# Performance work log

Hardware: AMD Instinct MI355X
Metric: run time of the kernel (lower is better)

Reference implementation:

```python
import jax, jax.numpy as jnp
import numpy as np

D_MODEL = 1024
N_HEADS = 16
HEAD_DIM = D_MODEL // N_HEADS  # 64
BATCH = 2
SEQ = 2048
THETA = 10000.0


def _rope_tables(theta, d_k, max_seq_len):
    # matches RoPE.__init__: d = theta**(2*arange(d_k//2)/d_k); t = s / d
    inv = theta ** (2.0 * jnp.arange(0, d_k // 2, dtype=jnp.float32) / d_k)  # [d_k//2]
    s = jnp.arange(max_seq_len, dtype=jnp.float32)[:, None]  # [S,1]
    t = s / inv[None, :]  # [S, d_k//2]
    return jnp.sin(t), jnp.cos(t)


def setup_inputs() -> dict:
    key = jax.random.key(0)
    ks = jax.random.split(key, 5)
    std = np.sqrt(2.0 / (D_MODEL + D_MODEL))
    x = jax.random.normal(ks[0], (BATCH, SEQ, D_MODEL), dtype=jnp.float32)
    Wq = jax.random.normal(ks[1], (D_MODEL, D_MODEL), dtype=jnp.float32) * std
    Wk = jax.random.normal(ks[2], (D_MODEL, D_MODEL), dtype=jnp.float32) * std
    Wv = jax.random.normal(ks[3], (D_MODEL, D_MODEL), dtype=jnp.float32) * std
    Wo = jax.random.normal(ks[4], (D_MODEL, D_MODEL), dtype=jnp.float32) * std
    token_positions = jnp.arange(SEQ, dtype=jnp.int64)
    rope_sin, rope_cos = _rope_tables(THETA, HEAD_DIM, SEQ)
    return {"x": x, "token_positions": token_positions, "Wq": Wq, "Wk": Wk,
            "Wv": Wv, "Wo": Wo, "rope_sin": rope_sin, "rope_cos": rope_cos}


def _apply_rope(x, sin, cos):
    # x: [B, H, S, d_k]; sin/cos: [S, d_k//2] (gathered by token_positions)
    x1 = x[..., ::2]
    x2 = x[..., 1::2]
    x_even = x1 * cos - x2 * sin
    x_odd = x1 * sin + x2 * cos
    # interleave back: stack on last dim then flatten
    return jnp.stack([x_even, x_odd], axis=-1).reshape(x.shape)


def reference(x, token_positions, Wq, Wk, Wv, Wo, rope_sin, rope_cos):
    b, s, _ = x.shape
    h, d = N_HEADS, HEAD_DIM

    def proj(W):
        y = jnp.einsum('oi,bsi->bso', W, x)
        return y.reshape(b, s, h, d).transpose(0, 2, 1, 3)  # [b, h, s, d]

    q = proj(Wq)
    k = proj(Wk)
    v = proj(Wv)

    sin = rope_sin[token_positions]  # [s, d//2]
    cos = rope_cos[token_positions]
    q = _apply_rope(q, sin, cos)
    k = _apply_rope(k, sin, cos)

    # causal scaled-dot-product attention (FlashAttention.apply(..., True))
    scale = 1.0 / jnp.sqrt(jnp.asarray(d, dtype=x.dtype))
    scores = jnp.einsum('bhqd,bhkd->bhqk', q, k) * scale
    causal = jnp.tril(jnp.ones((s, s), dtype=bool))
    scores = jnp.where(causal, scores, jnp.finfo(x.dtype).min)
    attn = jax.nn.softmax(scores, axis=-1)
    out = jnp.einsum('bhqk,bhkd->bhqd', attn, v)  # [b, h, s, d]
    out = out.transpose(0, 2, 1, 3).reshape(b, s, h * d)
    return jnp.einsum('oi,bsi->bso', Wo, out)
```

## Files before the change

kernel.cpp:

```cpp
#include <hip/hip_runtime.h>
#include <hip/hip_bf16.h>
#include <math.h>

#define BATCH   2
#define S_LEN   2048
#define DM      1024
#define NH      16
#define HD      64
#define MROWS   4096

typedef __hip_bfloat16 bf16;
typedef __attribute__((ext_vector_type(8))) short short8;
typedef __attribute__((ext_vector_type(4))) float float4v;

#define QSCALE 0.18033688011112043f

#define WC_VM0   0x0F70
#define WC_VM3   0x0F73
#define WC_VM4   0x0F74
#define WC_VM6   0x0F76
#define WC_VM8   0x0F78
#define WC_LGKM0 0xC07F

__device__ __forceinline__ short f2s(float x) {
    union { bf16 h; short s; } u; u.h = __float2bfloat16(x); return u.s;
}
__device__ __forceinline__ short8 load8(const void* p) {
    return *reinterpret_cast<const short8*>(p);
}
__device__ __forceinline__ void cvt8(const float* g, bf16* d) {
    float4v a = *reinterpret_cast<const float4v*>(g);
    float4v b = *reinterpret_cast<const float4v*>(g + 4);
    short8 r;
    r[0] = f2s(a[0]); r[1] = f2s(a[1]); r[2] = f2s(a[2]); r[3] = f2s(a[3]);
    r[4] = f2s(b[0]); r[5] = f2s(b[1]); r[6] = f2s(b[2]); r[7] = f2s(b[3]);
    *reinterpret_cast<short8*>(d) = r;
}
__device__ __forceinline__ void gll16(const void* g, void* l) {
    __builtin_amdgcn_global_load_lds(
        (const __attribute__((address_space(1))) unsigned int*)g,
        (__attribute__((address_space(3))) unsigned int*)l,
        16, 0, 0);
}
__device__ __forceinline__ unsigned pack2(float a, float b) {
    union { float f; unsigned u; } ua, ub;
    ua.f = a; ub.f = b;
    return ((ua.u + 0x8000u) >> 16) | ((ub.u + 0x8000u) & 0xFFFF0000u);
}

__global__ __launch_bounds__(256) void cvt_kernel(const float* __restrict__ x,
                                                  const float* __restrict__ wq,
                                                  const float* __restrict__ wk,
                                                  const float* __restrict__ wv,
                                                  const float* __restrict__ wo,
                                                  bf16* __restrict__ xb,
                                                  bf16* __restrict__ wqb,
                                                  bf16* __restrict__ wkb,
                                                  bf16* __restrict__ wvb,
                                                  bf16* __restrict__ wob) {
    const size_t i = ((size_t)blockIdx.x * 256 + threadIdx.x) * 8;
    const size_t NX = (size_t)MROWS * DM;
    const size_t NW = (size_t)DM * DM;
    if (i < NX)                { cvt8(x  + i,               xb  + i); }
    else if (i < NX + NW)      { cvt8(wq + (i - NX),        wqb + (i - NX)); }
    else if (i < NX + 2 * NW)  { cvt8(wk + (i - NX - NW),   wkb + (i - NX - NW)); }
    else if (i < NX + 3 * NW)  { cvt8(wv + (i - NX - 2*NW), wvb + (i - NX - 2*NW)); }
    else                       { cvt8(wo + (i - NX - 3*NW), wob + (i - NX - 3*NW)); }
}

__global__ __launch_bounds__(256) void qkv_gemm(const bf16* __restrict__ A,
                                                const bf16* __restrict__ Wqb,
                                                const bf16* __restrict__ Wkb,
                                                const bf16* __restrict__ Wvb,
                                                bf16* __restrict__ Qb, bf16* __restrict__ Kb,
                                                bf16* __restrict__ Vtb,
                                                const float* __restrict__ rsin,
                                                const float* __restrict__ rcos) {
    __shared__ short As[3][128 * 32];
    __shared__ short Bs[3][128 * 32];

    const int j    = threadIdx.x;
    const int w    = j >> 6;
    const int lane = j & 63;
    const int quad = lane >> 4;
    const int lid  = lane & 15;
    const int wm   = w & 1, wn = w >> 1;

    const int mb  = blockIdx.x * 128;
    const int sel = blockIdx.y >> 3;
    const int nb  = (blockIdx.y & 7) * 128;
    const bf16* W = (sel == 0) ? Wqb : (sel == 1) ? Wkb : Wvb;

    int sOff[2];
#pragma unroll
    for (int i = 0; i < 2; ++i) {
        const int idx = (i * 4 + w) * 64 + lane;
        const int r = idx >> 2;
        const int c = (idx & 3) ^ (r & 3) ^ ((r >> 2) & 3);
        sOff[i] = r * DM + c * 8;
    }
    const bf16* baseA = A + (size_t)mb * DM;
    const bf16* baseB = W + (size_t)nb * DM;

#pragma unroll
    for (int t = 0; t < 2; ++t) {
#pragma unroll
        for (int i = 0; i < 2; ++i) gll16(baseA + t * 32 + sOff[i], &As[t][(i * 4 + w) * 512]);
#pragma unroll
        for (int i = 0; i < 2; ++i) gll16(baseB + t * 32 + sOff[i], &Bs[t][(i * 4 + w) * 512]);
    }

    int aRd[4], bRd[4];
#pragma unroll
    for (int t = 0; t < 4; ++t) {
        const int ra = wm * 64 + t * 16 + lid;
        aRd[t] = ra * 32 + ((quad ^ (ra & 3) ^ ((ra >> 2) & 3)) * 8);
        const int rb = wn * 64 + t * 16 + lid;
        bRd[t] = rb * 32 + ((quad ^ (rb & 3) ^ ((rb >> 2) & 3)) * 8);
    }

    float4v acc[4][4] = {};
    int buf = 0;
    for (int it = 0; it < 32; ++it) {
        __builtin_amdgcn_s_barrier();
        if (it < 30) {
            const int k0 = (it + 2) * 32;
            const int b = (buf + 2 >= 3) ? buf - 1 : buf + 2;
#pragma unroll
            for (int i = 0; i < 2; ++i) gll16(baseA + k0 + sOff[i], &As[b][(i * 4 + w) * 512]);
#pragma unroll
            for (int i = 0; i < 2; ++i) gll16(baseB + k0 + sOff[i], &Bs[b][(i * 4 + w) * 512]);
            __builtin_amdgcn_s_waitcnt(WC_VM8);
        } else if (it == 30) {
            __builtin_amdgcn_s_waitcnt(WC_VM4);
        } else {
            __builtin_amdgcn_s_waitcnt(WC_VM0);
        }
        __builtin_amdgcn_s_barrier();

        const short* as = As[buf];
        const short* bs = Bs[buf];
        short8 af[4], bfr[4];
#pragma unroll
        for (int mt = 0; mt < 4; ++mt) af[mt] = load8(&as[aRd[mt]]);
#pragma unroll
        for (int nt = 0; nt < 4; ++nt) bfr[nt] = load8(&bs[bRd[nt]]);
#pragma unroll
        for (int mt = 0; mt < 4; ++mt)
#pragma unroll
            for (int nt = 0; nt < 4; ++nt)
                acc[mt][nt] = __builtin_amdgcn_mfma_f32_16x16x32_bf16(af[mt], bfr[nt], acc[mt][nt], 0, 0, 0);
        buf = (buf == 2) ? 0 : buf + 1;
    }

#pragma unroll
    for (int mt = 0; mt < 4; ++mt) {
#pragma unroll
        for (int nt = 0; nt < 4; ++nt) {
            const int n = nb + wn * 64 + nt * 16 + lid;
            const int h = n >> 6, d = n & 63;
#pragma unroll
            for (int r = 0; r < 4; ++r) {
                const int m = mb + wm * 64 + mt * 16 + quad * 4 + r;
                const int s = m & (S_LEN - 1), bi = m >> 11;
                float val = acc[mt][nt][r];
                if (sel == 0) val *= QSCALE;
                float par = __shfl_xor(val, 1, 64);
                if (sel == 2) {
                    Vtb[(((size_t)bi * NH + h) * HD + d) * S_LEN + s] = __float2bfloat16(val);
                } else {
                    const float sn = rsin[s * 32 + (d >> 1)];
                    const float cs = rcos[s * 32 + (d >> 1)];
                    const float v = ((d & 1) == 0) ? val * cs - par * sn
                                                   : par * sn + val * cs;
                    bf16* dst = (sel == 0) ? Qb : Kb;
                    dst[(((size_t)bi * NH + h) * S_LEN + s) * HD + d] = __float2bfloat16(v);
                }
            }
        }
    }
}

__global__ __launch_bounds__(256) void out_gemm(const bf16* __restrict__ A,
                                                const bf16* __restrict__ W,
                                                float* __restrict__ out) {
    __shared__ short As[3][128 * 32];
    __shared__ short Bs[3][64 * 32];

    const int j    = threadIdx.x;
    const int w    = j >> 6;
    const int lane = j & 63;
    const int quad = lane >> 4;
    const int lid  = lane & 15;

    const int mb = blockIdx.x * 128;
    const int nb = blockIdx.y * 64;

    int aOff[2], bOff;
#pragma unroll
    for (int i = 0; i < 2; ++i) {
        const int idx = (i * 4 + w) * 64 + lane;
        const int r = idx >> 2;
        const int c = (idx & 3) ^ (r & 3) ^ ((r >> 2) & 3);
        aOff[i] = r * DM + c * 8;
    }
    {
        const int idx = w * 64 + lane;
        const int r = idx >> 2;
        const int c = (idx & 3) ^ (r & 3) ^ ((r >> 2) & 3);
        bOff = r * DM + c * 8;
    }
    const bf16* baseA = A + (size_t)mb * DM;
    const bf16* baseB = W + (size_t)nb * DM;

#pragma unroll
    for (int t = 0; t < 2; ++t) {
#pragma unroll
        for (int i = 0; i < 2; ++i) gll16(baseA + t * 32 + aOff[i], &As[t][(i * 4 + w) * 512]);
        gll16(baseB + t * 32 + bOff, &Bs[t][w * 512]);
    }

    int aRd[2], bRd[4];
#pragma unroll
    for (int t = 0; t < 2; ++t) {
        const int ra = w * 32 + t * 16 + lid;
        aRd[t] = ra * 32 + ((quad ^ (ra & 3) ^ ((ra >> 2) & 3)) * 8);
    }
#pragma unroll
    for (int t = 0; t < 4; ++t) {
        const int rb = t * 16 + lid;
        bRd[t] = rb * 32 + ((quad ^ (rb & 3) ^ ((rb >> 2) & 3)) * 8);
    }

    float4v acc[2][4] = {};
    int buf = 0;
    for (int it = 0; it < 32; ++it) {
        __builtin_amdgcn_s_barrier();
        if (it < 30) {
            const int k0 = (it + 2) * 32;
            const int b = (buf + 2 >= 3) ? buf - 1 : buf + 2;
#pragma unroll
            for (int i = 0; i < 2; ++i) gll16(baseA + k0 + aOff[i], &As[b][(i * 4 + w) * 512]);
            gll16(baseB + k0 + bOff, &Bs[b][w * 512]);
            __builtin_amdgcn_s_waitcnt(WC_VM6);
        } else if (it == 30) {
            __builtin_amdgcn_s_waitcnt(WC_VM3);
        } else {
            __builtin_amdgcn_s_waitcnt(WC_VM0);
        }
        __builtin_amdgcn_s_barrier();

        const short* as = As[buf];
        const short* bs = Bs[buf];
        short8 af[2], bfr[4];
#pragma unroll
        for (int mt = 0; mt < 2; ++mt) af[mt] = load8(&as[aRd[mt]]);
#pragma unroll
        for (int nt = 0; nt < 4; ++nt) bfr[nt] = load8(&bs[bRd[nt]]);
#pragma unroll
        for (int mt = 0; mt < 2; ++mt)
#pragma unroll
            for (int nt = 0; nt < 4; ++nt)
                acc[mt][nt] = __builtin_amdgcn_mfma_f32_16x16x32_bf16(af[mt], bfr[nt], acc[mt][nt], 0, 0, 0);
        buf = (buf == 2) ? 0 : buf + 1;
    }

#pragma unroll
    for (int mt = 0; mt < 2; ++mt)
#pragma unroll
        for (int nt = 0; nt < 4; ++nt) {
            const int n = nb + nt * 16 + lid;
#pragma unroll
            for (int r = 0; r < 4; ++r) {
                const int m = mb + w * 32 + mt * 16 + quad * 4 + r;
                out[(size_t)m * DM + n] = acc[mt][nt][r];
            }
        }
}

__global__ __launch_bounds__(256) void flash6(const bf16* __restrict__ Q,
                                              const bf16* __restrict__ K,
                                              const bf16* __restrict__ Vt,
                                              bf16* __restrict__ att) {
    __shared__ short Ks[128 * 64];
    __shared__ short Vs[64 * 128];
    __shared__ short Pb[128 * 128];

    const int j    = threadIdx.x;
    const int w    = j >> 6;
    const int lane = j & 63;
    const int quad = lane >> 4;
    const int lid  = lane & 15;
    const int bh   = blockIdx.x;
    const int by   = blockIdx.y;
    const int qt   = (by < 8) ? (15 - by) : (by - 8);
    const int bi   = bh >> 4, h = bh & 15;
    const int qb   = qt * 128;

    const size_t bh_off = (size_t)bh * S_LEN * HD;
    const bf16* Qp = Q + bh_off;
    const bf16* Kp = K + bh_off;
    const bf16* Vp = Vt + bh_off;

    short8 aQ[2][2];
#pragma unroll
    for (int mm = 0; mm < 2; ++mm)
#pragma unroll
        for (int kf = 0; kf < 2; ++kf)
            aQ[mm][kf] = load8(Qp + (size_t)(qb + w * 32 + mm * 16 + lid) * HD + kf * 32 + quad * 8);

    int kOff[4], vOff[4];
#pragma unroll
    for (int i = 0; i < 4; ++i) {
        const int idx = (i * 4 + w) * 64 + lane;
        const int kr = idx >> 3, kc = (idx & 7) ^ (kr & 7);
        kOff[i] = kr * HD + kc * 8;
        const int vr = idx >> 4, vc = (idx & 15) ^ (vr & 15);
        vOff[i] = vr * S_LEN + vc * 8;
    }

    float4v accO[2][4] = {};
    float4v accS[2] = {};
    short8 ones;
#pragma unroll
    for (int t = 0; t < 8; ++t) ones[t] = (short)0x3F80;

    short8 kReg[4], vReg[4];
#pragma unroll
    for (int i = 0; i < 4; ++i) kReg[i] = load8(Kp + kOff[i]);
#pragma unroll
    for (int i = 0; i < 4; ++i) vReg[i] = load8(Vp + vOff[i]);

    const int nkt = qt + 1;
    for (int kti = 0; kti < nkt; ++kti) {
        __builtin_amdgcn_s_barrier();
#pragma unroll
        for (int i = 0; i < 4; ++i)
            *reinterpret_cast<short8*>(&Ks[(i * 4 + w) * 512 + lane * 8]) = kReg[i];
#pragma unroll
        for (int i = 0; i < 4; ++i)
            *reinterpret_cast<short8*>(&Vs[(i * 4 + w) * 512 + lane * 8]) = vReg[i];
        if (kti + 1 < nkt) {
            const int ktn = (kti + 1) * 128;
#pragma unroll
            for (int i = 0; i < 4; ++i) kReg[i] = load8(Kp + (size_t)ktn * HD + kOff[i]);
#pragma unroll
            for (int i = 0; i < 4; ++i) vReg[i] = load8(Vp + ktn + vOff[i]);
        }
        __builtin_amdgcn_s_waitcnt(WC_LGKM0);
        __builtin_amdgcn_s_barrier();

        const int kt = kti * 128;
        const bool diag = (kti == nkt - 1);

#pragma unroll
        for (int nt = 0; nt < 8; ++nt) {
            const int krow = nt * 16 + lid;
            short8 aK0 = load8(&Ks[krow * 64 + ((quad       ^ (lid & 7)) * 8)]);
            short8 aK1 = load8(&Ks[krow * 64 + (((4 + quad) ^ (lid & 7)) * 8)]);
#pragma unroll
            for (int mm = 0; mm < 2; ++mm) {
                float4v z = {};
                z = __builtin_amdgcn_mfma_f32_16x16x32_bf16(aK0, aQ[mm][0], z, 0, 0, 0);
                z = __builtin_amdgcn_mfma_f32_16x16x32_bf16(aK1, aQ[mm][1], z, 0, 0, 0);
                if (diag) {
                    const int qcol = qb + w * 32 + mm * 16 + lid;
#pragma unroll
                    for (int r = 0; r < 4; ++r)
                        if (kt + nt * 16 + quad * 4 + r > qcol) z[r] = -1e30f;
                }
                const float p0 = __builtin_amdgcn_exp2f(z[0]);
                const float p1 = __builtin_amdgcn_exp2f(z[1]);
                const float p2 = __builtin_amdgcn_exp2f(z[2]);
                const float p3 = __builtin_amdgcn_exp2f(z[3]);
                const int qrow = w * 32 + mm * 16 + lid;
                const int unit = (nt * 4 + quad) ^ ((lid & 7) * 2);
                uint2 pkd; pkd.x = pack2(p0, p1); pkd.y = pack2(p2, p3);
                *reinterpret_cast<uint2*>(&Pb[qrow * 128 + unit * 4]) = pkd;
            }
        }

        short8 aP[2][4];
#pragma unroll
        for (int mm = 0; mm < 2; ++mm) {
            const int qrow = w * 32 + mm * 16 + lid;
#pragma unroll
            for (int g = 0; g < 4; ++g) {
                const int u = (g * 8 + quad * 2) ^ ((lid & 7) * 2);
                aP[mm][g] = load8(&Pb[qrow * 128 + u * 4]);
                accS[mm] = __builtin_amdgcn_mfma_f32_16x16x32_bf16(aP[mm][g], ones, accS[mm], 0, 0, 0);
            }
        }
#pragma unroll
        for (int dt = 0; dt < 4; ++dt) {
#pragma unroll
            for (int g = 0; g < 4; ++g) {
                short8 bV = load8(&Vs[(dt * 16 + lid) * 128 + (((g * 4 + quad) ^ lid) * 8)]);
#pragma unroll
                for (int mm = 0; mm < 2; ++mm)
                    accO[mm][dt] = __builtin_amdgcn_mfma_f32_16x16x32_bf16(aP[mm][g], bV, accO[mm][dt], 0, 0, 0);
            }
        }
    }

#pragma unroll
    for (int mm = 0; mm < 2; ++mm) {
#pragma unroll
        for (int r = 0; r < 4; ++r) {
            const float inv = 1.0f / accS[mm][r];
            const int q = qb + w * 32 + mm * 16 + quad * 4 + r;
#pragma unroll
            for (int dt = 0; dt < 4; ++dt) {
                const int d = dt * 16 + lid;
                att[((size_t)bi * S_LEN + q) * DM + h * HD + d] =
                    __float2bfloat16(accO[mm][dt][r] * inv);
            }
        }
    }
}

extern "C" void kernel_launch(void* const* d_in, const int* in_sizes, int n_in,
                              void* d_out, int out_size, void* d_ws, size_t ws_size,
                              hipStream_t stream) {
    const float* x    = (const float*)d_in[0];
    const float* Wq   = (const float*)d_in[2];
    const float* Wk   = (const float*)d_in[3];
    const float* Wv   = (const float*)d_in[4];
    const float* Wo   = (const float*)d_in[5];
    const float* rsin = (const float*)d_in[6];
    const float* rcos = (const float*)d_in[7];
    float* out = (float*)d_out;

    char* ws = (char*)d_ws;
    const size_t MB = 1024 * 1024;
    bf16* Qb  = (bf16*)(ws + 0 * MB);
    bf16* Kb  = (bf16*)(ws + 8 * MB);
    bf16* Vtb = (bf16*)(ws + 16 * MB);
    bf16* xb  = (bf16*)(ws + 24 * MB);
    bf16* Wqb = (bf16*)(ws + 32 * MB);
    bf16* Wkb = (bf16*)(ws + 34 * MB);
    bf16* Wvb = (bf16*)(ws + 36 * MB);
    bf16* Wob = (bf16*)(ws + 38 * MB);
    bf16* atb = xb;

    cvt_kernel<<<4096, 256, 0, stream>>>(x, Wq, Wk, Wv, Wo, xb, Wqb, Wkb, Wvb, Wob);
    qkv_gemm<<<dim3(MROWS / 128, 24), 256, 0, stream>>>(xb, Wqb, Wkb, Wvb, Qb, Kb, Vtb, rsin, rcos);
    flash6<<<dim3(BATCH * NH, 16), 256, 0, stream>>>(Qb, Kb, Vtb, atb);
    out_gemm<<<dim3(MROWS / 128, DM / 64), 256, 0, stream>>>(atb, Wob, out);
}
```

Baseline: 183.8 us.

## Enlarge QKV GEMM tile to 256x256 with 8 waves and double buffering

Rewrites the QKV projection GEMM to use 256x256 output tiles with 512 threads and a K step of 64, replacing the 128x128 triple-buffered scheme. Each wave computes a 128x64 sub-tile with fragment loads interleaved between MFMA groups, and the MFMA sections are wrapped in s_setprio. Larger tiles raise arithmetic intensity and cut global and LDS traffic per FLOP. In exchange the grid shrinks to 192 blocks, which may underfill the CUs, and the larger register and LDS footprint (128KB LDS per block) limits occupancy.

```diff
diff --git a/kernel.cpp b/kernel.cpp
--- a/kernel.cpp
+++ b/kernel.cpp
@@ -68,113 +68,156 @@
     else                       { cvt8(wo + (i - NX - 3*NW), wob + (i - NX - 3*NW)); }
 }
 
-__global__ __launch_bounds__(256) void qkv_gemm(const bf16* __restrict__ A,
-                                                const bf16* __restrict__ Wqb,
-                                                const bf16* __restrict__ Wkb,
-                                                const bf16* __restrict__ Wvb,
-                                                bf16* __restrict__ Qb, bf16* __restrict__ Kb,
-                                                bf16* __restrict__ Vtb,
-                                                const float* __restrict__ rsin,
-                                                const float* __restrict__ rcos) {
-    __shared__ short As[3][128 * 32];
-    __shared__ short Bs[3][128 * 32];
-
-    const int j    = threadIdx.x;
-    const int w    = j >> 6;
-    const int lane = j & 63;
+__global__ __launch_bounds__(512, 2) void qkv_gemm(const bf16* __restrict__ A,
+                                                   const bf16* __restrict__ Wqb,
+                                                   const bf16* __restrict__ Wkb,
+                                                   const bf16* __restrict__ Wvb,
+                                                   bf16* __restrict__ Qb, bf16* __restrict__ Kb,
+                                                   bf16* __restrict__ Vtb,
+                                                   const float* __restrict__ rsin,
+                                                   const float* __restrict__ rcos) {
+    __shared__ __align__(16) short As[2][256 * 64];
+    __shared__ __align__(16) short Bs[2][256 * 64];
+
+    const int tid  = threadIdx.x;
+    const int wid  = tid >> 6;
+    const int lane = tid & 63;
     const int quad = lane >> 4;
     const int lid  = lane & 15;
-    const int wm   = w & 1, wn = w >> 1;
-
-    const int mb  = blockIdx.x * 128;
-    const int sel = blockIdx.y >> 3;
-    const int nb  = (blockIdx.y & 7) * 128;
+    const int wm   = wid >> 2;
+    const int wn   = wid & 3;
+
+    const int mb        = blockIdx.x * 256;
+    const int nGlobBase = blockIdx.y * 256;
+    const int sel       = nGlobBase >> 10;
+    const int n0        = nGlobBase & 1023;
     const bf16* W = (sel == 0) ? Wqb : (sel == 1) ? Wkb : Wvb;
 
-    int sOff[2];
-#pragma unroll
-    for (int i = 0; i < 2; ++i) {
-        const int idx = (i * 4 + w) * 64 + lane;
-        const int r = idx >> 2;
-        const int c = (idx & 3) ^ (r & 3) ^ ((r >> 2) & 3);
-        sOff[i] = r * DM + c * 8;
-    }
     const bf16* baseA = A + (size_t)mb * DM;
-    const bf16* baseB = W + (size_t)nb * DM;
-
-#pragma unroll
-    for (int t = 0; t < 2; ++t) {
-#pragma unroll
-        for (int i = 0; i < 2; ++i) gll16(baseA + t * 32 + sOff[i], &As[t][(i * 4 + w) * 512]);
-#pragma unroll
-        for (int i = 0; i < 2; ++i) gll16(baseB + t * 32 + sOff[i], &Bs[t][(i * 4 + w) * 512]);
-    }
-
-    int aRd[4], bRd[4];
-#pragma unroll
-    for (int t = 0; t < 4; ++t) {
-        const int ra = wm * 64 + t * 16 + lid;
-        aRd[t] = ra * 32 + ((quad ^ (ra & 3) ^ ((ra >> 2) & 3)) * 8);
-        const int rb = wn * 64 + t * 16 + lid;
-        bRd[t] = rb * 32 + ((quad ^ (rb & 3) ^ ((rb >> 2) & 3)) * 8);
-    }
-
-    float4v acc[4][4] = {};
-    int buf = 0;
-    for (int it = 0; it < 32; ++it) {
-        __builtin_amdgcn_s_barrier();
-        if (it < 30) {
-            const int k0 = (it + 2) * 32;
-            const int b = (buf + 2 >= 3) ? buf - 1 : buf + 2;
-#pragma unroll
-            for (int i = 0; i < 2; ++i) gll16(baseA + k0 + sOff[i], &As[b][(i * 4 + w) * 512]);
-#pragma unroll
-            for (int i = 0; i < 2; ++i) gll16(baseB + k0 + sOff[i], &Bs[b][(i * 4 + w) * 512]);
+    const bf16* baseB = W + (size_t)n0 * DM;
+
+    int sOff[4], lBase[4];
+#pragma unroll
+    for (int i = 0; i < 4; ++i) {
+        const int u = i * 512 + tid;
+        const int r = u >> 3;
+        const int c = (u & 7) ^ (r & 7);
+        sOff[i]  = r * DM + c * 8;
+        lBase[i] = (i * 512 + wid * 64) * 8;
+    }
+
+#pragma unroll
+    for (int i = 0; i < 4; ++i) gll16(baseA + sOff[i], &As[0][lBase[i]]);
+#pragma unroll
+    for (int i = 0; i < 4; ++i) gll16(baseB + sOff[i], &Bs[0][lBase[i]]);
+
+    const int aBase = (wm * 128 + lid) * 64 + (quad ^ (lid & 7)) * 8;
+    const int bBase = (wn * 64  + lid) * 64 + (quad ^ (lid & 7)) * 8;
+
+    float4v acc[8][4] = {};
+
+    for (int t = 0; t < 16; ++t) {
+        __builtin_amdgcn_s_barrier();
+        if (t < 15) {
+            const bf16* pa = baseA + (t + 1) * 64;
+            const bf16* pb = baseB + (t + 1) * 64;
+            short* an = As[(t + 1) & 1];
+            short* bn = Bs[(t + 1) & 1];
+#pragma unroll
+            for (int i = 0; i < 4; ++i) gll16(pa + sOff[i], &an[lBase[i]]);
+#pragma unroll
+            for (int i = 0; i < 4; ++i) gll16(pb + sOff[i], &bn[lBase[i]]);
             __builtin_amdgcn_s_waitcnt(WC_VM8);
-        } else if (it == 30) {
-            __builtin_amdgcn_s_waitcnt(WC_VM4);
         } else {
             __builtin_amdgcn_s_waitcnt(WC_VM0);
         }
         __builtin_amdgcn_s_barrier();
 
-        const short* as = As[buf];
-        const short* bs = Bs[buf];
-        short8 af[4], bfr[4];
-#pragma unroll
-        for (int mt = 0; mt < 4; ++mt) af[mt] = load8(&as[aRd[mt]]);
-#pragma unroll
-        for (int nt = 0; nt < 4; ++nt) bfr[nt] = load8(&bs[bRd[nt]]);
-#pragma unroll
-        for (int mt = 0; mt < 4; ++mt)
-#pragma unroll
-            for (int nt = 0; nt < 4; ++nt)
-                acc[mt][nt] = __builtin_amdgcn_mfma_f32_16x16x32_bf16(af[mt], bfr[nt], acc[mt][nt], 0, 0, 0);
-        buf = (buf == 2) ? 0 : buf + 1;
-    }
-
-#pragma unroll
-    for (int mt = 0; mt < 4; ++mt) {
-#pragma unroll
-        for (int nt = 0; nt < 4; ++nt) {
-            const int n = nb + wn * 64 + nt * 16 + lid;
-            const int h = n >> 6, d = n & 63;
+        const short* as = As[t & 1];
+        const short* bs = Bs[t & 1];
+
+        short8 aF[4][2], bA[2][2], bB[2][2];
+
+#pragma unroll
+        for (int mf = 0; mf < 4; ++mf)
+#pragma unroll
+            for (int ks = 0; ks < 2; ++ks)
+                aF[mf][ks] = load8(&as[(aBase + mf * 1024) ^ (ks * 32)]);
+#pragma unroll
+        for (int nf = 0; nf < 2; ++nf)
+#pragma unroll
+            for (int ks = 0; ks < 2; ++ks)
+                bA[nf][ks] = load8(&bs[(bBase + nf * 1024) ^ (ks * 32)]);
+        __builtin_amdgcn_s_setprio(1);
+#pragma unroll
+        for (int mf = 0; mf < 4; ++mf)
+#pragma unroll
+            for (int nf = 0; nf < 2; ++nf)
+#pragma unroll
+                for (int ks = 0; ks < 2; ++ks)
+                    acc[mf][nf] = __builtin_amdgcn_mfma_f32_16x16x32_bf16(aF[mf][ks], bA[nf][ks], acc[mf][nf], 0, 0, 0);
+        __builtin_amdgcn_s_setprio(0);
+
+#pragma unroll
+        for (int nf = 0; nf < 2; ++nf)
+#pragma unroll
+            for (int ks = 0; ks < 2; ++ks)
+                bB[nf][ks] = load8(&bs[(bBase + (2 + nf) * 1024) ^ (ks * 32)]);
+        __builtin_amdgcn_s_setprio(1);
+#pragma unroll
+        for (int mf = 0; mf < 4; ++mf)
+#pragma unroll
+            for (int nf = 0; nf < 2; ++nf)
+#pragma unroll
+                for (int ks = 0; ks < 2; ++ks)
+                    acc[mf][2 + nf] = __builtin_amdgcn_mfma_f32_16x16x32_bf16(aF[mf][ks], bB[nf][ks], acc[mf][2 + nf], 0, 0, 0);
+        __builtin_amdgcn_s_setprio(0);
+
+#pragma unroll
+        for (int mf = 0; mf < 4; ++mf)
+#pragma unroll
+            for (int ks = 0; ks < 2; ++ks)
+                aF[mf][ks] = load8(&as[(aBase + (4 + mf) * 1024) ^ (ks * 32)]);
+        __builtin_amdgcn_s_setprio(1);
+#pragma unroll
+        for (int mf = 0; mf < 4; ++mf)
+#pragma unroll
+            for (int nf = 0; nf < 2; ++nf)
+#pragma unroll
+                for (int ks = 0; ks < 2; ++ks)
+                    acc[4 + mf][nf] = __builtin_amdgcn_mfma_f32_16x16x32_bf16(aF[mf][ks], bA[nf][ks], acc[4 + mf][nf], 0, 0, 0);
+#pragma unroll
+        for (int mf = 0; mf < 4; ++mf)
+#pragma unroll
+            for (int nf = 0; nf < 2; ++nf)
+#pragma unroll
+                for (int ks = 0; ks < 2; ++ks)
+                    acc[4 + mf][2 + nf] = __builtin_amdgcn_mfma_f32_16x16x32_bf16(aF[mf][ks], bB[nf][ks], acc[4 + mf][2 + nf], 0, 0, 0);
+        __builtin_amdgcn_s_setprio(0);
+    }
+
+    const int hh = (n0 >> 6) + wn;
+#pragma unroll
+    for (int mf = 0; mf < 8; ++mf) {
+#pragma unroll
+        for (int nf = 0; nf < 4; ++nf) {
+            const int d = nf * 16 + lid;
 #pragma unroll
             for (int r = 0; r < 4; ++r) {
-                const int m = mb + wm * 64 + mt * 16 + quad * 4 + r;
+                const int m = mb + wm * 128 + mf * 16 + quad * 4 + r;
                 const int s = m & (S_LEN - 1), bi = m >> 11;
-                float val = acc[mt][nt][r];
+                float val = acc[mf][nf][r];
                 if (sel == 0) val *= QSCALE;
                 float par = __shfl_xor(val, 1, 64);
                 if (sel == 2) {
-                    Vtb[(((size_t)bi * NH + h) * HD + d) * S_LEN + s] = __float2bfloat16(val);
+                    Vtb[(((size_t)bi * NH + hh) * HD + d) * S_LEN + s] = __float2bfloat16(val);
                 } else {
                     const float sn = rsin[s * 32 + (d >> 1)];
                     const float cs = rcos[s * 32 + (d >> 1)];
                     const float v = ((d & 1) == 0) ? val * cs - par * sn
                                                    : par * sn + val * cs;
                     bf16* dst = (sel == 0) ? Qb : Kb;
-                    dst[(((size_t)bi * NH + h) * S_LEN + s) * HD + d] = __float2bfloat16(v);
+                    dst[(((size_t)bi * NH + hh) * S_LEN + s) * HD + d] = __float2bfloat16(v);
                 }
             }
         }
@@ -444,7 +487,7 @@
     bf16* atb = xb;
 
     cvt_kernel<<<4096, 256, 0, stream>>>(x, Wq, Wk, Wv, Wo, xb, Wqb, Wkb, Wvb, Wob);
-    qkv_gemm<<<dim3(MROWS / 128, 24), 256, 0, stream>>>(xb, Wqb, Wkb, Wvb, Qb, Kb, Vtb, rsin, rcos);
+    qkv_gemm<<<dim3(MROWS / 256, 12), 512, 0, stream>>>(xb, Wqb, Wkb, Wvb, Qb, Kb, Vtb, rsin, rcos);
     flash6<<<dim3(BATCH * NH, 16), 256, 0, stream>>>(Qb, Kb, Vtb, atb);
     out_gemm<<<dim3(MROWS / 128, DM / 64), 256, 0, stream>>>(atb, Wob, out);
 }
```

Result: slower. 197.3 us (+7.4%).
